# Optimization experiments

Measured on AMD Instinct MI355X. Metric: run time of the kernel, lower is better.

## Reference

```python
import jax, jax.numpy as jnp
import numpy as np

N = 100000        # nodes
E_HALF = 1600000  # directed edges before symmetrization
NFEAT, NHID, NOUT = 512, 256, 64
K = 10            # Chebyshev order


def setup_inputs() -> dict:
    key = jax.random.key(0)
    k_feat, k_src, k_dst, k_w1, k_w2, k_tmp = jax.random.split(key, 6)
    feature = jax.random.normal(k_feat, (N, NFEAT), jnp.float32)
    src = jax.random.randint(k_src, (E_HALF,), 0, N, jnp.int32)
    dst = jax.random.randint(k_dst, (E_HALF,), 0, N, jnp.int32)
    # symmetrize so the adjacency (and hence the normalized Laplacian) is symmetric
    edge_index = jnp.stack([jnp.concatenate([src, dst]), jnp.concatenate([dst, src])])  # [2, 2*E_HALF]
    W1 = jax.random.normal(k_w1, (NHID, NFEAT), jnp.float32) / np.sqrt(NFEAT)
    b1 = jnp.zeros((NHID,), jnp.float32)
    W2 = jax.random.normal(k_w2, (NOUT, NHID), jnp.float32) / np.sqrt(NHID)
    b2 = jnp.zeros((NOUT,), jnp.float32)
    # ChebnetII_prop.temp is initialized to 1.0; jitter so relu/grads are non-trivial
    temp = 1.0 + 0.1 * jax.random.normal(k_tmp, (K + 1,), jnp.float32)
    return {"feature": feature, "W1": W1, "b1": b1, "W2": W2, "b2": b2,
            "temp": temp, "edge_index": edge_index}


def _cheb_coeffs(temp):
    # coe[i] = 2/(K+1) * sum_j relu(temp)[j] * T_i(x_j),  x_j = cos((K-j+0.5)*pi/(K+1))
    # and T_i(cos(theta)) = cos(i*theta)
    coe_tmp = jax.nn.relu(temp)
    j = jnp.arange(K + 1, dtype=temp.dtype)
    theta = (K - j + 0.5) * jnp.pi / (K + 1)          # [K+1]
    i = jnp.arange(K + 1, dtype=temp.dtype)
    T = jnp.cos(i[:, None] * theta[None, :])           # [K+1, K+1] Chebyshev eval table
    return (2.0 / (K + 1)) * (T @ coe_tmp)             # [K+1]


def reference(feature, W1, b1, W2, b2, temp, edge_index):
    # dense MLP part (dropout is identity in eval mode)
    x = jax.nn.relu(feature @ W1.T + b1)               # [N, NHID]
    x = x @ W2.T + b2                                  # [N, NOUT]

    # ChebnetII_prop: propagate with L_tilde = L_sym - I = -D^{-1/2} A D^{-1/2}
    row, col = edge_index[0], edge_index[1]
    w = jnp.ones(row.shape, x.dtype)                   # unit edge weights (binary adjacency)
    deg = jax.ops.segment_sum(w, row, num_segments=N)  # [N]
    dinv = jnp.where(deg > 0, jax.lax.rsqrt(jnp.maximum(deg, 1.0)), 0.0)
    norm = -dinv[row] * w * dinv[col]                  # [E] edge weights of (L - I)

    def prop(v):  # v: [N, NOUT] -> (L - I) @ v via gather/scatter
        return jax.ops.segment_sum(norm[:, None] * v[col], row, num_segments=N)

    coe = _cheb_coeffs(temp)
    Tx0 = x
    Tx1 = prop(x)
    out = coe[0] / 2.0 * Tx0 + coe[1] * Tx1
    for i in range(2, K + 1):                          # Chebyshev recursion (K fixed, small)
        Tx2 = 2.0 * prop(Tx1) - Tx0
        out = out + coe[i] * Tx2
        Tx0, Tx1 = Tx1, Tx2
    return out                                         # [N, NOUT]
```

## Files before the change

### kernel.cpp

```cpp
#include <hip/hip_runtime.h>

#define K_ORDER 10
#define NFEAT 512
#define NHID 256
#define NOUT 64
#define PI_F 3.14159265358979323846f
#define SCAN_CHUNK 2048

typedef __bf16 bf16x8 __attribute__((ext_vector_type(8)));
typedef unsigned short ushort8 __attribute__((ext_vector_type(8)));
typedef float f32x4 __attribute__((ext_vector_type(4)));

__device__ __forceinline__ float bf2f(unsigned short u) {
    union { unsigned int i; float f; } x;
    x.i = ((unsigned int)u) << 16;
    return x.f;
}

__global__ void detect_kernel(const unsigned short* __restrict__ temp, int* __restrict__ flag) {
    if (threadIdx.x == 0 && blockIdx.x == 0) {
        int cnt = 0;
        for (int i = 0; i < K_ORDER + 1; ++i) {
            unsigned short s = temp[i];
            if (s >= 0x3E00 && s < 0x4080) cnt++;
        }
        flag[0] = (cnt >= 9) ? 1 : 0;
    }
}


__global__ void count_deg_kernel(const int* __restrict__ row, int* __restrict__ deg, int e) {
    int i = blockIdx.x * blockDim.x + threadIdx.x;
    if (i < e) atomicAdd(&deg[row[i]], 1);
}

__global__ void dinv_kernel(const int* __restrict__ deg, float* __restrict__ dinv, int n) {
    int i = blockIdx.x * blockDim.x + threadIdx.x;
    if (i < n) {
        int d = deg[i];
        dinv[i] = (d > 0) ? rsqrtf((float)d) : 0.0f;
    }
}


__global__ __launch_bounds__(256) void partial_sum_kernel(const int* __restrict__ deg,
                                                          int* __restrict__ bsum, int n) {
    __shared__ int ws[4];
    int b = blockIdx.x, t = threadIdx.x;
    int base = b * SCAN_CHUNK + t * 8;
    int s = 0;
    #pragma unroll
    for (int j = 0; j < 8; ++j) { int i = base + j; if (i < n) s += deg[i]; }
    #pragma unroll
    for (int m = 1; m < 64; m <<= 1) s += __shfl_xor(s, m, 64);
    if ((t & 63) == 0) ws[t >> 6] = s;
    __syncthreads();
    if (t == 0) bsum[b] = ws[0] + ws[1] + ws[2] + ws[3];
}

__global__ void scan_small_kernel(const int* __restrict__ bsum, int* __restrict__ boff,
                                  int* __restrict__ rowptr, int nb, int n) {
    int t = threadIdx.x;
    int v = (t < nb) ? bsum[t] : 0;
    int x = v;
    #pragma unroll
    for (int m = 1; m < 64; m <<= 1) { int y = __shfl_up(x, m, 64); if (t >= m) x += y; }
    if (t < nb) boff[t] = x - v;
    if (t == 63) rowptr[n] = x;
}

__global__ __launch_bounds__(256) void scan_apply_kernel(const int* __restrict__ deg,
                                                         const int* __restrict__ boff,
                                                         int* __restrict__ rowptr,
                                                         int* __restrict__ cursor, int n) {
    __shared__ int wtot[4];
    __shared__ int woff_s[4];
    int b = blockIdx.x, t = threadIdx.x;
    int lane = t & 63, wid = t >> 6;
    int base = b * SCAN_CHUNK + t * 8;
    int v[8], s[8];
    int run = 0;
    #pragma unroll
    for (int j = 0; j < 8; ++j) {
        int i = base + j;
        v[j] = (i < n) ? deg[i] : 0;
        run += v[j];
        s[j] = run;
    }
    int tsum = run;
    int x = tsum;
    #pragma unroll
    for (int m = 1; m < 64; m <<= 1) { int y = __shfl_up(x, m, 64); if (lane >= m) x += y; }
    int texcl = x - tsum;
    if (lane == 63) wtot[wid] = x;
    __syncthreads();
    if (t == 0) {
        int r = 0;
        #pragma unroll
        for (int w = 0; w < 4; ++w) { woff_s[w] = r; r += wtot[w]; }
    }
    __syncthreads();
    int ebase = boff[b] + woff_s[wid] + texcl;
    #pragma unroll
    for (int j = 0; j < 8; ++j) {
        int i = base + j;
        if (i < n) { int ex = ebase + s[j] - v[j]; rowptr[i] = ex; cursor[i] = ex; }
    }
}

__global__ void scatter_kernel(const int* __restrict__ row, const int* __restrict__ col,
                               int* __restrict__ cursor, int* __restrict__ cols_s, int e) {
    int i = blockIdx.x * blockDim.x + threadIdx.x;
    if (i < e) {
        int p = atomicAdd(&cursor[row[i]], 1);
        cols_s[p] = col[i];
    }
}


__global__ void coef_kernel(const void* __restrict__ temp, const int* __restrict__ flag,
                            float* __restrict__ coe) {
    int i = threadIdx.x;
    bool isbf = flag[0] != 0;
    if (i <= K_ORDER) {
        float s = 0.0f;
        #pragma unroll
        for (int j = 0; j <= K_ORDER; ++j) {
            float t = isbf ? bf2f(((const unsigned short*)temp)[j]) : ((const float*)temp)[j];
            t = fmaxf(t, 0.0f);
            float theta = ((float)(K_ORDER - j) + 0.5f) * PI_F / (float)(K_ORDER + 1);
            s += cosf((float)i * theta) * t;
        }
        coe[i] = (2.0f / (float)(K_ORDER + 1)) * s;
    }
}


template<int BN, bool RELU, bool A_FLAGGED>
__global__ __launch_bounds__(256) void gemm_kernel(const void* __restrict__ A,
                                                   const void* __restrict__ B,
                                                   const void* __restrict__ bias,
                                                   const int* __restrict__ flag,
                                                   unsigned short* __restrict__ C,
                                                   int M, int Kdim, int ldc) {
    constexpr int BM = 128, BK = 32;
    constexpr int FN = BN / 32;
    constexpr int LDT = BK + 8;
    __shared__ unsigned short lds_a[BM * LDT] __attribute__((aligned(16)));
    __shared__ unsigned short lds_b[BN * LDT] __attribute__((aligned(16)));

    const bool isbf = flag[0] != 0;
    int tid = threadIdx.x;
    int lane = tid & 63, wid = tid >> 6;
    int row0 = blockIdx.x * BM;
    int col0 = blockIdx.y * BN;
    int wrow = (wid >> 1) * (BM / 2);
    int wcol = (wid & 1) * (BN / 2);

    f32x4 acc[4][FN] = {};

    for (int k0 = 0; k0 < Kdim; k0 += BK) {
        #pragma unroll
        for (int it = 0; it < (BM * BK / 8) / 256; ++it) {
            int idx = it * 256 + tid;
            int r = idx >> 2;
            int kc = (idx & 3) * 8;
            int gr = row0 + r; if (gr >= M) gr = M - 1;
            size_t base = (size_t)gr * Kdim + k0 + kc;
            if (!A_FLAGGED || isbf) {
                *(ushort8*)&lds_a[r * LDT + kc] = *(const ushort8*)((const unsigned short*)A + base);
            } else {
                const float* Af = (const float*)A;
                f32x4 lo = *(const f32x4*)(Af + base);
                f32x4 hi = *(const f32x4*)(Af + base + 4);
                bf16x8 v;
                #pragma unroll
                for (int j = 0; j < 4; ++j) { v[j] = (__bf16)lo[j]; v[j + 4] = (__bf16)hi[j]; }
                *(bf16x8*)&lds_a[r * LDT + kc] = v;
            }
        }
        #pragma unroll
        for (int it = 0; it < (BN * BK / 8) / 256; ++it) {
            int idx = it * 256 + tid;
            int r = idx >> 2;
            int kc = (idx & 3) * 8;
            size_t base = (size_t)(col0 + r) * Kdim + k0 + kc;
            if (isbf) {
                *(ushort8*)&lds_b[r * LDT + kc] = *(const ushort8*)((const unsigned short*)B + base);
            } else {
                const float* Bf = (const float*)B;
                f32x4 lo = *(const f32x4*)(Bf + base);
                f32x4 hi = *(const f32x4*)(Bf + base + 4);
                bf16x8 v;
                #pragma unroll
                for (int j = 0; j < 4; ++j) { v[j] = (__bf16)lo[j]; v[j + 4] = (__bf16)hi[j]; }
                *(bf16x8*)&lds_b[r * LDT + kc] = v;
            }
        }
        __syncthreads();

        int kq = (lane >> 4) * 8;
        bf16x8 af[4];
        bf16x8 bfr[FN];
        #pragma unroll
        for (int mi = 0; mi < 4; ++mi)
            af[mi] = *(bf16x8*)&lds_a[(wrow + mi * 16 + (lane & 15)) * LDT + kq];
        #pragma unroll
        for (int ni = 0; ni < FN; ++ni)
            bfr[ni] = *(bf16x8*)&lds_b[(wcol + ni * 16 + (lane & 15)) * LDT + kq];
        #pragma unroll
        for (int mi = 0; mi < 4; ++mi)
            #pragma unroll
            for (int ni = 0; ni < FN; ++ni)
                acc[mi][ni] = __builtin_amdgcn_mfma_f32_16x16x32_bf16(af[mi], bfr[ni],
                                                                      acc[mi][ni], 0, 0, 0);
        __syncthreads();
    }

    #pragma unroll
    for (int mi = 0; mi < 4; ++mi) {
        #pragma unroll
        for (int ni = 0; ni < FN; ++ni) {
            #pragma unroll
            for (int rg = 0; rg < 4; ++rg) {
                int grow = row0 + wrow + mi * 16 + (lane >> 4) * 4 + rg;
                int gcol = col0 + wcol + ni * 16 + (lane & 15);
                if (grow < M) {
                    float bb = isbf ? bf2f(((const unsigned short*)bias)[gcol])
                                    : ((const float*)bias)[gcol];
                    float vv = acc[mi][ni][rg] + bb;
                    if (RELU) vv = fmaxf(vv, 0.0f);
                    __bf16 h = (__bf16)vv;
                    C[(size_t)grow * ldc + gcol] = *(unsigned short*)&h;
                }
            }
        }
    }
}


__global__ __launch_bounds__(256) void prop_kernel(const unsigned short* __restrict__ vsrc,
                                                   unsigned short* __restrict__ tdst,
                                                   float* __restrict__ outacc,
                                                   const int* __restrict__ rowptr,
                                                   const int* __restrict__ cols,
                                                   const float* __restrict__ dinv,
                                                   const float* __restrict__ coe,
                                                   int mode, int ci, int n) {
    int lane = threadIdx.x & 63;
    int r = blockIdx.x * 4 + (threadIdx.x >> 6);
    if (r >= n) return;
    int fc = lane & 7;
    int sub = lane >> 3;
    int e0 = rowptr[r], e1 = rowptr[r + 1];
    float acc[8] = {};
    for (int e = e0; e < e1; e += 8) {
        int ee = e + sub;
        bool valid = ee < e1;
        int c = valid ? cols[ee] : 0;
        float w = valid ? dinv[c] : 0.0f;
        ushort8 vv = *(const ushort8*)&vsrc[(size_t)c * NOUT + fc * 8];
        #pragma unroll
        for (int j = 0; j < 8; ++j)
            acc[j] = fmaf(w, bf2f(vv[j]), acc[j]);
    }
    #pragma unroll
    for (int m = 8; m < 64; m <<= 1)
        #pragma unroll
        for (int j = 0; j < 8; ++j)
            acc[j] += __shfl_xor(acc[j], m, 64);

    if (lane < 8) {
        float dr = -dinv[r];
        size_t idx = (size_t)r * NOUT + lane * 8;
        float P[8];
        #pragma unroll
        for (int j = 0; j < 8; ++j) P[j] = dr * acc[j];
        if (mode == 0) {
            ushort8 v0 = *(const ushort8*)&vsrc[idx];
            ushort8 hout;
            #pragma unroll
            for (int j = 0; j < 8; ++j) {
                __bf16 h = (__bf16)P[j];
                hout[j] = *(unsigned short*)&h;
            }
            *(ushort8*)&tdst[idx] = hout;
            #pragma unroll
            for (int j = 0; j < 8; ++j)
                outacc[idx + j] = coe[0] * 0.5f * bf2f(v0[j]) + coe[1] * P[j];
        } else {
            ushort8 t0v = *(const ushort8*)&tdst[idx];
            ushort8 hout;
            float t2a[8];
            #pragma unroll
            for (int j = 0; j < 8; ++j) {
                float t2 = 2.0f * P[j] - bf2f(t0v[j]);
                t2a[j] = t2;
                __bf16 h = (__bf16)t2;
                hout[j] = *(unsigned short*)&h;
            }
            *(ushort8*)&tdst[idx] = hout;
            #pragma unroll
            for (int j = 0; j < 8; ++j)
                outacc[idx + j] += coe[ci] * t2a[j];
        }
    }
}

__global__ void convert_kernel(const float* __restrict__ in, const int* __restrict__ flag,
                               void* __restrict__ out, int n) {
    int i = blockIdx.x * blockDim.x + threadIdx.x;
    bool isbf = flag[0] != 0;
    if (i < n) {
        float v = in[i];
        if (isbf) {
            __bf16 h = (__bf16)v;
            ((unsigned short*)out)[i] = *(unsigned short*)&h;
        } else {
            ((float*)out)[i] = v;
        }
    }
}


extern "C" void kernel_launch(void* const* d_in, const int* in_sizes, int n_in,
                              void* d_out, int out_size, void* d_ws, size_t ws_size,
                              hipStream_t stream) {
    const void* feature = d_in[0];
    const void* W1      = d_in[1];
    const void* b1      = d_in[2];
    const void* W2      = d_in[3];
    const void* b2      = d_in[4];
    const void* temp    = d_in[5];
    const int* edge_index = (const int*)d_in[6];

    const int N = in_sizes[0] / NFEAT;
    const int E = in_sizes[6] / 2;
    const int* row = edge_index;
    const int* col = edge_index + E;
    const int nb = (N + SCAN_CHUNK - 1) / SCAN_CHUNK;

    char* base = (char*)d_ws;
    size_t off = 0;
    auto alloc = [&](size_t bytes) -> char* {
        char* p = base + off;
        off = (off + bytes + 255) & ~(size_t)255;
        return p;
    };
    int*   flag   = (int*)  alloc(4);
    float* coe    = (float*)alloc(64);
    int*   bsum   = (int*)  alloc(256);
    int*   boff   = (int*)  alloc(256);
    float* dinv   = (float*)alloc((size_t)N * 4);
    int*   deg    = (int*)  alloc((size_t)N * 4);
    int*   rowptr = (int*)  alloc((size_t)(N + 1) * 4);
    int*   cursor = (int*)  alloc((size_t)(N + 1) * 4);
    char*  R      = alloc((size_t)N * NHID * 2);
    unsigned short* xhid = (unsigned short*)R;
    int*   colss  = (int*)R;
    float* outacc = (float*)(R + (size_t)E * 4);
    unsigned short* t_a = (unsigned short*)alloc((size_t)N * NOUT * 2);
    unsigned short* t_b = (unsigned short*)alloc((size_t)N * NOUT * 2);

    detect_kernel<<<1, 64, 0, stream>>>((const unsigned short*)temp, flag);
    coef_kernel<<<1, 64, 0, stream>>>(temp, flag, coe);

    gemm_kernel<128, true, true><<<dim3((N + 127) / 128, NHID / 128), 256, 0, stream>>>(
        feature, W1, b1, flag, xhid, N, NFEAT, NHID);
    gemm_kernel<64, false, false><<<dim3((N + 127) / 128, 1), 256, 0, stream>>>(
        xhid, W2, b2, flag, t_a, N, NHID, NOUT);

    hipMemsetAsync(deg, 0, (size_t)N * 4, stream);
    count_deg_kernel<<<(E + 255) / 256, 256, 0, stream>>>(row, deg, E);
    dinv_kernel<<<(N + 255) / 256, 256, 0, stream>>>(deg, dinv, N);
    partial_sum_kernel<<<nb, 256, 0, stream>>>(deg, bsum, N);
    scan_small_kernel<<<1, 64, 0, stream>>>(bsum, boff, rowptr, nb, N);
    scan_apply_kernel<<<nb, 256, 0, stream>>>(deg, boff, rowptr, cursor, N);
    scatter_kernel<<<(E + 255) / 256, 256, 0, stream>>>(row, col, cursor, colss, E);

    int pb = (N + 3) / 4;
    prop_kernel<<<pb, 256, 0, stream>>>(t_a, t_b, outacc, rowptr, colss, dinv, coe, 0, 0, N);
    unsigned short* src = t_b;
    unsigned short* dst = t_a;
    for (int i = 2; i <= K_ORDER; ++i) {
        prop_kernel<<<pb, 256, 0, stream>>>(src, dst, outacc, rowptr, colss, dinv, coe, 1, i, N);
        unsigned short* tmp = src; src = dst; dst = tmp;
    }

    convert_kernel<<<(N * NOUT + 255) / 256, 256, 0, stream>>>(outacc, flag, d_out, N * NOUT);
}
```

Baseline: 1.598 ms.

## Build CSR via two-pass bucketed binning instead of per-row atomic scatter

Replaces the single scatter that did a global atomic per edge on a per-row cursor with a two-pass bucketed sort. The first pass bins edges into 128-row buckets with global atomics and packs the local row index and column into one word. The second pass places edges within each bucket using shared-memory atomics. The aim is better write locality for the CSR column array, at the cost of an extra pass over the edges and heavy atomic contention on the bucket counters.

```diff
diff --git a/kernel.cpp b/kernel.cpp
--- a/kernel.cpp
+++ b/kernel.cpp
@@ -6,6 +6,8 @@
 #define NOUT 64
 #define PI_F 3.14159265358979323846f
 #define SCAN_CHUNK 2048
+#define BUCKET_SHIFT 7
+#define BUCKET_ROWS 128
 
 typedef __bf16 bf16x8 __attribute__((ext_vector_type(8)));
 typedef unsigned short ushort8 __attribute__((ext_vector_type(8)));
@@ -71,8 +73,7 @@
 
 __global__ __launch_bounds__(256) void scan_apply_kernel(const int* __restrict__ deg,
                                                          const int* __restrict__ boff,
-                                                         int* __restrict__ rowptr,
-                                                         int* __restrict__ cursor, int n) {
+                                                         int* __restrict__ rowptr, int n) {
     __shared__ int wtot[4];
     __shared__ int woff_s[4];
     int b = blockIdx.x, t = threadIdx.x;
@@ -104,16 +105,51 @@
     #pragma unroll
     for (int j = 0; j < 8; ++j) {
         int i = base + j;
-        if (i < n) { int ex = ebase + s[j] - v[j]; rowptr[i] = ex; cursor[i] = ex; }
-    }
-}
-
-__global__ void scatter_kernel(const int* __restrict__ row, const int* __restrict__ col,
-                               int* __restrict__ cursor, int* __restrict__ cols_s, int e) {
+        if (i < n) rowptr[i] = ebase + s[j] - v[j];
+    }
+}
+
+
+__global__ void bcur_init_kernel(const int* __restrict__ rowptr, int* __restrict__ bcur,
+                                 int nb, int n) {
+    int b = blockIdx.x * blockDim.x + threadIdx.x;
+    if (b < nb) {
+        int r = b * BUCKET_ROWS;
+        if (r > n) r = n;
+        bcur[b] = rowptr[r];
+    }
+}
+
+__global__ void bin_pass1_kernel(const int* __restrict__ row, const int* __restrict__ col,
+                                 int* __restrict__ bcur, unsigned int* __restrict__ packed,
+                                 int e) {
     int i = blockIdx.x * blockDim.x + threadIdx.x;
     if (i < e) {
-        int p = atomicAdd(&cursor[row[i]], 1);
-        cols_s[p] = col[i];
+        int r = row[i];
+        int c = col[i];
+        int b = r >> BUCKET_SHIFT;
+        int p = atomicAdd(&bcur[b], 1);
+        packed[p] = ((unsigned int)(r & (BUCKET_ROWS - 1)) << 17) | (unsigned int)c;
+    }
+}
+
+__global__ __launch_bounds__(256) void bin_pass2_kernel(const unsigned int* __restrict__ packed,
+                                                        const int* __restrict__ rowptr,
+                                                        int* __restrict__ cols_s, int n) {
+    __shared__ int lcur[BUCKET_ROWS];
+    int b = blockIdx.x, t = threadIdx.x;
+    int row0 = b * BUCKET_ROWS;
+    int rhi = row0 + BUCKET_ROWS; if (rhi > n) rhi = n;
+    if (t < BUCKET_ROWS && row0 + t < n) lcur[t] = rowptr[row0 + t];
+    __syncthreads();
+    int start = rowptr[row0];
+    int end = rowptr[rhi];
+    for (int e = start + t; e < end; e += 256) {
+        unsigned int pk = packed[e];
+        int rl = pk >> 17;
+        int c = (int)(pk & 0x1FFFFu);
+        int p = atomicAdd(&lcur[rl], 1);
+        cols_s[p] = c;
     }
 }
 
@@ -338,7 +374,8 @@
     const int E = in_sizes[6] / 2;
     const int* row = edge_index;
     const int* col = edge_index + E;
-    const int nb = (N + SCAN_CHUNK - 1) / SCAN_CHUNK;
+    const int nb_scan = (N + SCAN_CHUNK - 1) / SCAN_CHUNK;
+    const int nb_bkt  = (N + BUCKET_ROWS - 1) / BUCKET_ROWS;
 
     char* base = (char*)d_ws;
     size_t off = 0;
@@ -351,14 +388,15 @@
     float* coe    = (float*)alloc(64);
     int*   bsum   = (int*)  alloc(256);
     int*   boff   = (int*)  alloc(256);
+    int*   bcur   = (int*)  alloc((size_t)(nb_bkt + 1) * 4);
     float* dinv   = (float*)alloc((size_t)N * 4);
     int*   deg    = (int*)  alloc((size_t)N * 4);
     int*   rowptr = (int*)  alloc((size_t)(N + 1) * 4);
-    int*   cursor = (int*)  alloc((size_t)(N + 1) * 4);
     char*  R      = alloc((size_t)N * NHID * 2);
     unsigned short* xhid = (unsigned short*)R;
     int*   colss  = (int*)R;
     float* outacc = (float*)(R + (size_t)E * 4);
+    unsigned int* packed = (unsigned int*)(R + (size_t)E * 4 + (size_t)N * NOUT * 4);
     unsigned short* t_a = (unsigned short*)alloc((size_t)N * NOUT * 2);
     unsigned short* t_b = (unsigned short*)alloc((size_t)N * NOUT * 2);
 
@@ -373,10 +411,12 @@
     hipMemsetAsync(deg, 0, (size_t)N * 4, stream);
     count_deg_kernel<<<(E + 255) / 256, 256, 0, stream>>>(row, deg, E);
     dinv_kernel<<<(N + 255) / 256, 256, 0, stream>>>(deg, dinv, N);
-    partial_sum_kernel<<<nb, 256, 0, stream>>>(deg, bsum, N);
-    scan_small_kernel<<<1, 64, 0, stream>>>(bsum, boff, rowptr, nb, N);
-    scan_apply_kernel<<<nb, 256, 0, stream>>>(deg, boff, rowptr, cursor, N);
-    scatter_kernel<<<(E + 255) / 256, 256, 0, stream>>>(row, col, cursor, colss, E);
+    partial_sum_kernel<<<nb_scan, 256, 0, stream>>>(deg, bsum, N);
+    scan_small_kernel<<<1, 64, 0, stream>>>(bsum, boff, rowptr, nb_scan, N);
+    scan_apply_kernel<<<nb_scan, 256, 0, stream>>>(deg, boff, rowptr, N);
+    bcur_init_kernel<<<(nb_bkt + 255) / 256, 256, 0, stream>>>(rowptr, bcur, nb_bkt, N);
+    bin_pass1_kernel<<<(E + 255) / 256, 256, 0, stream>>>(row, col, bcur, packed, E);
+    bin_pass2_kernel<<<nb_bkt, 256, 0, stream>>>(packed, rowptr, colss, N);
 
     int pb = (N + 3) / 4;
     prop_kernel<<<pb, 256, 0, stream>>>(t_a, t_b, outacc, rowptr, colss, dinv, coe, 0, 0, N);
```

Result: slower. 2.122 ms (+32.8%).
